# Kernel tuning notes

Measured on AMD Instinct MI355X. Metric: run time of the kernel, lower is better.

## Reference

```python
import jax, jax.numpy as jnp
import numpy as np

N_NODES = 100000


def gcn_conv(x, W, b, src, dst, num_nodes):
    # GCNConv with self-loops and symmetric normalization (PyG defaults).
    h = x @ W  # [N, F_out]
    ones = jnp.ones(src.shape[0], dtype=x.dtype)
    deg = jax.ops.segment_sum(ones, dst, num_segments=num_nodes) + 1.0  # +1 self-loop
    dinv = jax.lax.rsqrt(deg)  # deg^{-1/2}
    norm = dinv[src] * dinv[dst]  # [E]
    msg = h[src] * norm[:, None]  # gather + scale, [E, F_out]
    agg = jax.ops.segment_sum(msg, dst, num_segments=num_nodes)
    agg = agg + h * (dinv * dinv)[:, None]  # self-loop term: dinv[i]*dinv[i]
    return agg + b


def setup_inputs() -> dict:
    key = jax.random.key(0)
    k = jax.random.split(key, 6)
    in_c, hid_c, out_c = 64, 64, 32
    E = 1600000
    x = jax.random.normal(k[0], (N_NODES, in_c), dtype=jnp.float32)
    edge_index = jax.random.randint(k[1], (2, E), 0, N_NODES, dtype=jnp.int32)
    W1 = jax.random.normal(k[2], (in_c, hid_c), dtype=jnp.float32) / np.sqrt(in_c)
    b1 = jnp.zeros((hid_c,), dtype=jnp.float32)
    W2 = jax.random.normal(k[3], (hid_c, out_c), dtype=jnp.float32) / np.sqrt(hid_c)
    b2 = jnp.zeros((out_c,), dtype=jnp.float32)
    return {"x": x, "edge_index": edge_index, "W1": W1, "b1": b1, "W2": W2, "b2": b2}


def reference(x, edge_index, W1, b1, W2, b2):
    src, dst = edge_index[0], edge_index[1]
    h = jax.nn.relu(gcn_conv(x, W1, b1, src, dst, N_NODES))
    # dropout is identity in inference mode
    h = gcn_conv(h, W2, b2, src, dst, N_NODES)
    return jax.nn.log_softmax(h, axis=1)
```

## Files before the change

### kernel.cpp

```cpp
#include <hip/hip_runtime.h>
#include <hip/hip_bf16.h>


constexpr int SCAN_CHUNK = 1024;

__device__ __forceinline__ unsigned short f2bf(float f) {
    unsigned u = __float_as_uint(f);
    return (unsigned short)((u + 0x7FFF + ((u >> 16) & 1)) >> 16);
}
__device__ __forceinline__ float bf2f(unsigned short b) {
    return __uint_as_float((unsigned)b << 16);
}

__global__ __launch_bounds__(256) void k_zero(int* __restrict__ p, int n) {
    int i = blockIdx.x * 256 + threadIdx.x;
    if (i < n) p[i] = 0;
}

__global__ __launch_bounds__(256) void k_hist_rank(const int* __restrict__ dst,
                                                   int* __restrict__ cnt,
                                                   int* __restrict__ rank, int E) {
    int e = blockIdx.x * 256 + threadIdx.x;
    if (e < E) rank[e] = atomicAdd(&cnt[dst[e]], 1);
}

__global__ __launch_bounds__(256) void k_scan1(const int* __restrict__ cnt,
                                               int* __restrict__ bsum, int N) {
    __shared__ int sm[256];
    const int t = threadIdx.x;
    const long base = (long)blockIdx.x * SCAN_CHUNK + t * 4;
    int s = 0;
    #pragma unroll
    for (int k = 0; k < 4; ++k) { long i = base + k; if (i < N) s += cnt[i]; }
    sm[t] = s; __syncthreads();
    for (int off = 128; off > 0; off >>= 1) {
        if (t < off) sm[t] += sm[t + off];
        __syncthreads();
    }
    if (t == 0) bsum[blockIdx.x] = sm[0];
}

__global__ __launch_bounds__(256) void k_scan2(const int* __restrict__ bsum,
                                               int* __restrict__ bofs, int nb) {
    __shared__ int sm[256];
    const int t = threadIdx.x;
    const int v = (t < nb) ? bsum[t] : 0;
    sm[t] = v; __syncthreads();
    for (int off = 1; off < 256; off <<= 1) {
        int u = (t >= off) ? sm[t - off] : 0;
        __syncthreads();
        sm[t] += u;
        __syncthreads();
    }
    if (t < nb) bofs[t] = sm[t] - v;
}

__global__ __launch_bounds__(256) void k_scan3(const int* __restrict__ cnt,
                                               const int* __restrict__ bofs,
                                               int* __restrict__ offs,
                                               float* __restrict__ dinv, int N) {
    __shared__ int sm[256];
    const int t = threadIdx.x;
    const long base = (long)blockIdx.x * SCAN_CHUNK + t * 4;
    int c[4]; int s = 0;
    #pragma unroll
    for (int k = 0; k < 4; ++k) { long i = base + k; c[k] = (i < N) ? cnt[i] : 0; s += c[k]; }
    sm[t] = s; __syncthreads();
    for (int off = 1; off < 256; off <<= 1) {
        int u = (t >= off) ? sm[t - off] : 0;
        __syncthreads();
        sm[t] += u;
        __syncthreads();
    }
    int run = bofs[blockIdx.x] + (sm[t] - s);
    #pragma unroll
    for (int k = 0; k < 4; ++k) {
        long i = base + k;
        if (i < N) {
            offs[i] = run;
            dinv[i] = rsqrtf((float)c[k] + 1.0f);
            run += c[k];
        }
    }
}

__global__ __launch_bounds__(256) void k_fill(const int* __restrict__ src,
                                              const int* __restrict__ dst,
                                              const int* __restrict__ rank,
                                              const int* __restrict__ offs,
                                              int* __restrict__ slots, int E) {
    int e = blockIdx.x * 256 + threadIdx.x;
    if (e >= E) return;
    const int pos = offs[dst[e]] + rank[e];
    __builtin_nontemporal_store(src[e], &slots[pos]);
}

template<int IN_C, int OUT_C, bool TRANS_IN>
__global__ __launch_bounds__(256) void k_mm(const float* __restrict__ A,
                                            const float* __restrict__ W,
                                            const float* __restrict__ bin,
                                            unsigned short* __restrict__ out,
                                            int n_rows) {
    constexpr int C4   = OUT_C / 4;
    constexpr int ROWS = 256 / C4;
    __shared__ float Ws[IN_C][OUT_C];
    __shared__ float xs[ROWS][IN_C + 1];
    __shared__ float bs[IN_C];

    const int tid = threadIdx.x;
    for (int i = tid; i < IN_C * OUT_C; i += 256)
        Ws[i / OUT_C][i % OUT_C] = W[i];
    if (tid < IN_C) bs[tid] = TRANS_IN ? bin[tid] : 0.0f;

    const int c4 = (tid % C4) * 4;
    const int rl = tid / C4;
    const int tiles = (n_rows + ROWS - 1) / ROWS;

    for (int t = blockIdx.x; t < tiles; t += gridDim.x) {
        const int r0 = t * ROWS;
        __syncthreads();
        for (int i = tid; i < ROWS * IN_C; i += 256) {
            int r = i / IN_C, k = i % IN_C;
            float v = 0.0f;
            if (r0 + r < n_rows) {
                v = A[(long)(r0 + r) * IN_C + k];
                if (TRANS_IN) v = fmaxf(v + bs[k], 0.0f);
            }
            xs[r][k] = v;
        }
        __syncthreads();

        float4 acc = {0.f, 0.f, 0.f, 0.f};
        #pragma unroll
        for (int k = 0; k < IN_C; ++k) {
            const float a = xs[rl][k];
            const float4 w4 = *reinterpret_cast<const float4*>(&Ws[k][c4]);
            acc.x += a * w4.x; acc.y += a * w4.y;
            acc.z += a * w4.z; acc.w += a * w4.w;
        }
        const int row = r0 + rl;
        if (row < n_rows) {
            ushort4 o;
            o.x = f2bf(acc.x); o.y = f2bf(acc.y);
            o.z = f2bf(acc.z); o.w = f2bf(acc.w);
            *reinterpret_cast<ushort4*>(&out[(long)row * OUT_C + c4]) = o;
        }
    }
}

__global__ __launch_bounds__(256) void k_agg64(const int* __restrict__ offs,
                                               const int* __restrict__ cnt,
                                               const int* __restrict__ slots,
                                               const float* __restrict__ dinv,
                                               const unsigned short* __restrict__ h,
                                               float* __restrict__ agg, int N) {
    const int wid  = threadIdx.x >> 6;
    const int lane = threadIdx.x & 63;
    const int grp  = lane >> 4;
    const int c4   = (lane & 15) * 4;
    const int node = blockIdx.x * 4 + wid;
    if (node >= N) return;
    const int beg = offs[node], deg = cnt[node];
    const float dd = dinv[node];
    float4 acc = {0.f, 0.f, 0.f, 0.f};
    for (int j0 = 0; j0 < deg; j0 += 64) {
        const int m = min(64, deg - j0);
        int sv = 0; float dv = 0.f;
        if (lane < m) { sv = slots[beg + j0 + lane]; dv = dinv[sv]; }
        #pragma unroll 4
        for (int jj = 0; jj < m; jj += 4) {
            const int idx = jj + grp;
            const int   s = __shfl(sv, idx);
            const float w = __shfl(dv, idx) * dd;
            if (idx < m) {
                const ushort4 hv = *reinterpret_cast<const ushort4*>(&h[(long)s * 64 + c4]);
                acc.x += w * bf2f(hv.x); acc.y += w * bf2f(hv.y);
                acc.z += w * bf2f(hv.z); acc.w += w * bf2f(hv.w);
            }
        }
    }
    #pragma unroll
    for (int off = 16; off <= 32; off <<= 1) {
        acc.x += __shfl_xor(acc.x, off); acc.y += __shfl_xor(acc.y, off);
        acc.z += __shfl_xor(acc.z, off); acc.w += __shfl_xor(acc.w, off);
    }
    if (lane < 16) {
        const ushort4 hv = *reinterpret_cast<const ushort4*>(&h[(long)node * 64 + c4]);
        const float w = dd * dd;
        acc.x += w * bf2f(hv.x); acc.y += w * bf2f(hv.y);
        acc.z += w * bf2f(hv.z); acc.w += w * bf2f(hv.w);
        *reinterpret_cast<float4*>(&agg[(long)node * 64 + c4]) = acc;
    }
}

__global__ __launch_bounds__(256) void k_agg32_lsm(const int* __restrict__ offs,
                                                   const int* __restrict__ cnt,
                                                   const int* __restrict__ slots,
                                                   const float* __restrict__ dinv,
                                                   const unsigned short* __restrict__ h,
                                                   const float* __restrict__ b2,
                                                   float* __restrict__ out, int N) {
    const int wid  = threadIdx.x >> 6;
    const int lane = threadIdx.x & 63;
    const int grp  = lane >> 3;
    const int c4   = (lane & 7) * 4;
    const int node = blockIdx.x * 4 + wid;
    if (node >= N) return;
    const int beg = offs[node], deg = cnt[node];
    const float dd = dinv[node];
    float4 acc = {0.f, 0.f, 0.f, 0.f};
    for (int j0 = 0; j0 < deg; j0 += 64) {
        const int m = min(64, deg - j0);
        int sv = 0; float dv = 0.f;
        if (lane < m) { sv = slots[beg + j0 + lane]; dv = dinv[sv]; }
        #pragma unroll 2
        for (int jj = 0; jj < m; jj += 8) {
            const int idx = jj + grp;
            const int   s = __shfl(sv, idx);
            const float w = __shfl(dv, idx) * dd;
            if (idx < m) {
                const ushort4 hv = *reinterpret_cast<const ushort4*>(&h[(long)s * 32 + c4]);
                acc.x += w * bf2f(hv.x); acc.y += w * bf2f(hv.y);
                acc.z += w * bf2f(hv.z); acc.w += w * bf2f(hv.w);
            }
        }
    }
    #pragma unroll
    for (int off = 8; off <= 32; off <<= 1) {
        acc.x += __shfl_xor(acc.x, off); acc.y += __shfl_xor(acc.y, off);
        acc.z += __shfl_xor(acc.z, off); acc.w += __shfl_xor(acc.w, off);
    }
    const ushort4 hv = *reinterpret_cast<const ushort4*>(&h[(long)node * 32 + c4]);
    const float4 bv = *reinterpret_cast<const float4*>(&b2[c4]);
    const float w = dd * dd;
    float4 v;
    v.x = acc.x + w * bf2f(hv.x) + bv.x; v.y = acc.y + w * bf2f(hv.y) + bv.y;
    v.z = acc.z + w * bf2f(hv.z) + bv.z; v.w = acc.w + w * bf2f(hv.w) + bv.w;
    float mx = fmaxf(fmaxf(v.x, v.y), fmaxf(v.z, v.w));
    #pragma unroll
    for (int off = 1; off < 8; off <<= 1) mx = fmaxf(mx, __shfl_xor(mx, off));
    float4 ev;
    ev.x = __expf(v.x - mx); ev.y = __expf(v.y - mx);
    ev.z = __expf(v.z - mx); ev.w = __expf(v.w - mx);
    float ss = ev.x + ev.y + ev.z + ev.w;
    #pragma unroll
    for (int off = 1; off < 8; off <<= 1) ss += __shfl_xor(ss, off);
    const float lg = mx + __logf(ss);
    if (lane < 8) {
        float4 o;
        o.x = v.x - lg; o.y = v.y - lg; o.z = v.z - lg; o.w = v.w - lg;
        *reinterpret_cast<float4*>(&out[(long)node * 32 + c4]) = o;
    }
}

extern "C" void kernel_launch(void* const* d_in, const int* in_sizes, int n_in,
                              void* d_out, int out_size, void* d_ws, size_t ws_size,
                              hipStream_t stream) {
    const float* x  = (const float*)d_in[0];
    const int*   ei = (const int*)  d_in[1];
    const float* W1 = (const float*)d_in[2];
    const float* b1 = (const float*)d_in[3];
    const float* W2 = (const float*)d_in[4];
    const float* b2 = (const float*)d_in[5];
    float* out = (float*)d_out;

    const int N = in_sizes[0] / 64;
    const int E = in_sizes[1] / 2;
    const int* src = ei;
    const int* dst = ei + E;

    auto align = [](long v) { return (v + 63) & ~63L; };
    char* wsb = (char*)d_ws;
    long o = 0;
    int*   cnt    = (int*)(wsb + o * 4); o = align(o + N);
    int*   offs   = (int*)(wsb + o * 4); o = align(o + N);
    int*   bsum   = (int*)(wsb + o * 4); o = align(o + 256);
    int*   bofs   = (int*)(wsb + o * 4); o = align(o + 256);
    float* dinv   = (float*)(wsb + o * 4); o = align(o + N);
    int*   slots  = (int*)(wsb + o * 4); o = align(o + E);
    unsigned short* h1 = (unsigned short*)(wsb + o * 4); o = align(o + (long)N * 32);
    float* agg1   = (float*)(wsb + o * 4); o = align(o + (long)N * 64);
    unsigned short* h2 = h1;
    int*   rank   = (int*)h1;

    const int B = 256;
    auto cdiv = [](long a, long b) { return (int)((a + b - 1) / b); };
    const int nb = cdiv(N, SCAN_CHUNK);

    k_zero     <<<cdiv(N, B), B, 0, stream>>>(cnt, N);
    k_hist_rank<<<cdiv(E, B), B, 0, stream>>>(dst, cnt, rank, E);
    k_scan1    <<<nb, B, 0, stream>>>(cnt, bsum, N);
    k_scan2    <<<1,  B, 0, stream>>>(bsum, bofs, nb);
    k_scan3    <<<nb, B, 0, stream>>>(cnt, bofs, offs, dinv, N);
    k_fill     <<<cdiv(E, B), B, 0, stream>>>(src, dst, rank, offs, slots, E);

    k_mm<64, 64, false><<<2048, B, 0, stream>>>(x, W1, b1, h1, N);
    k_agg64<<<cdiv(N, 4), B, 0, stream>>>(offs, cnt, slots, dinv, h1, agg1, N);

    k_mm<64, 32, true><<<2048, B, 0, stream>>>(agg1, W2, b1, h2, N);
    k_agg32_lsm<<<cdiv(N, 4), B, 0, stream>>>(offs, cnt, slots, dinv, h2, b2, out, N);
}
```

Measured before the change: 353.8 us.

## Privatize degree histogram into eight copies to reduce atomic contention

The degree histogram is split into eight per-block-group copies, so each edge's atomicAdd targets one of eight counters chosen by block index. The scan kernels sum the copies and write a per-copy offset table, and the fill kernel uses that offset plus the rank to place each source. The aim is to spread contended atomics across more addresses. In exchange the zeroing, scan and offset traffic grows eightfold over N, and each edge in the fill stage does a scattered lookup into an array eight times larger.

```diff
diff --git a/kernel.cpp b/kernel.cpp
--- a/kernel.cpp
+++ b/kernel.cpp
@@ -3,6 +3,7 @@
 
 
 constexpr int SCAN_CHUNK = 1024;
+constexpr int NCPY = 8;
 
 __device__ __forceinline__ unsigned short f2bf(float f) {
     unsigned u = __float_as_uint(f);
@@ -12,26 +13,34 @@
     return __uint_as_float((unsigned)b << 16);
 }
 
-__global__ __launch_bounds__(256) void k_zero(int* __restrict__ p, int n) {
-    int i = blockIdx.x * 256 + threadIdx.x;
+__global__ __launch_bounds__(256) void k_zero(int* __restrict__ p, long n) {
+    long i = (long)blockIdx.x * 256 + threadIdx.x;
     if (i < n) p[i] = 0;
 }
 
-__global__ __launch_bounds__(256) void k_hist_rank(const int* __restrict__ dst,
-                                                   int* __restrict__ cnt,
-                                                   int* __restrict__ rank, int E) {
+__global__ __launch_bounds__(256) void k_hist_rank8(const int* __restrict__ dst,
+                                                    int* __restrict__ cnt8,
+                                                    int* __restrict__ rank,
+                                                    int N, int E) {
     int e = blockIdx.x * 256 + threadIdx.x;
-    if (e < E) rank[e] = atomicAdd(&cnt[dst[e]], 1);
-}
-
-__global__ __launch_bounds__(256) void k_scan1(const int* __restrict__ cnt,
+    if (e >= E) return;
+    const int c = blockIdx.x & (NCPY - 1);
+    rank[e] = atomicAdd(&cnt8[(long)c * N + dst[e]], 1);
+}
+
+__global__ __launch_bounds__(256) void k_scan1(const int* __restrict__ cnt8,
                                                int* __restrict__ bsum, int N) {
     __shared__ int sm[256];
     const int t = threadIdx.x;
     const long base = (long)blockIdx.x * SCAN_CHUNK + t * 4;
     int s = 0;
     #pragma unroll
-    for (int k = 0; k < 4; ++k) { long i = base + k; if (i < N) s += cnt[i]; }
+    for (int k = 0; k < 4; ++k) {
+        long i = base + k;
+        if (i < N)
+            #pragma unroll
+            for (int c = 0; c < NCPY; ++c) s += cnt8[(long)c * N + i];
+    }
     sm[t] = s; __syncthreads();
     for (int off = 128; off > 0; off >>= 1) {
         if (t < off) sm[t] += sm[t + off];
@@ -55,16 +64,26 @@
     if (t < nb) bofs[t] = sm[t] - v;
 }
 
-__global__ __launch_bounds__(256) void k_scan3(const int* __restrict__ cnt,
+__global__ __launch_bounds__(256) void k_scan3(const int* __restrict__ cnt8,
                                                const int* __restrict__ bofs,
                                                int* __restrict__ offs,
+                                               int* __restrict__ deg,
+                                               int* __restrict__ copyoff,
                                                float* __restrict__ dinv, int N) {
     __shared__ int sm[256];
     const int t = threadIdx.x;
     const long base = (long)blockIdx.x * SCAN_CHUNK + t * 4;
-    int c[4]; int s = 0;
-    #pragma unroll
-    for (int k = 0; k < 4; ++k) { long i = base + k; c[k] = (i < N) ? cnt[i] : 0; s += c[k]; }
+    int c8[4][NCPY]; int tot[4]; int s = 0;
+    #pragma unroll
+    for (int k = 0; k < 4; ++k) {
+        long i = base + k; tot[k] = 0;
+        #pragma unroll
+        for (int c = 0; c < NCPY; ++c) {
+            c8[k][c] = (i < N) ? cnt8[(long)c * N + i] : 0;
+            tot[k] += c8[k][c];
+        }
+        s += tot[k];
+    }
     sm[t] = s; __syncthreads();
     for (int off = 1; off < 256; off <<= 1) {
         int u = (t >= off) ? sm[t - off] : 0;
@@ -78,20 +97,26 @@
         long i = base + k;
         if (i < N) {
             offs[i] = run;
-            dinv[i] = rsqrtf((float)c[k] + 1.0f);
-            run += c[k];
-        }
-    }
-}
-
-__global__ __launch_bounds__(256) void k_fill(const int* __restrict__ src,
-                                              const int* __restrict__ dst,
-                                              const int* __restrict__ rank,
-                                              const int* __restrict__ offs,
-                                              int* __restrict__ slots, int E) {
+            deg[i]  = tot[k];
+            dinv[i] = rsqrtf((float)tot[k] + 1.0f);
+            int a = run;
+            #pragma unroll
+            for (int c = 0; c < NCPY; ++c) { copyoff[(long)c * N + i] = a; a += c8[k][c]; }
+            run += tot[k];
+        }
+    }
+}
+
+__global__ __launch_bounds__(256) void k_fill8(const int* __restrict__ src,
+                                               const int* __restrict__ dst,
+                                               const int* __restrict__ rank,
+                                               const int* __restrict__ copyoff,
+                                               int* __restrict__ slots,
+                                               int N, int E) {
     int e = blockIdx.x * 256 + threadIdx.x;
     if (e >= E) return;
-    const int pos = offs[dst[e]] + rank[e];
+    const int c = blockIdx.x & (NCPY - 1);
+    const int pos = copyoff[(long)c * N + dst[e]] + rank[e];
     __builtin_nontemporal_store(src[e], &slots[pos]);
 }
 
@@ -149,7 +174,7 @@
 }
 
 __global__ __launch_bounds__(256) void k_agg64(const int* __restrict__ offs,
-                                               const int* __restrict__ cnt,
+                                               const int* __restrict__ deg,
                                                const int* __restrict__ slots,
                                                const float* __restrict__ dinv,
                                                const unsigned short* __restrict__ h,
@@ -160,11 +185,11 @@
     const int c4   = (lane & 15) * 4;
     const int node = blockIdx.x * 4 + wid;
     if (node >= N) return;
-    const int beg = offs[node], deg = cnt[node];
+    const int beg = offs[node], dg = deg[node];
     const float dd = dinv[node];
     float4 acc = {0.f, 0.f, 0.f, 0.f};
-    for (int j0 = 0; j0 < deg; j0 += 64) {
-        const int m = min(64, deg - j0);
+    for (int j0 = 0; j0 < dg; j0 += 64) {
+        const int m = min(64, dg - j0);
         int sv = 0; float dv = 0.f;
         if (lane < m) { sv = slots[beg + j0 + lane]; dv = dinv[sv]; }
         #pragma unroll 4
@@ -194,7 +219,7 @@
 }
 
 __global__ __launch_bounds__(256) void k_agg32_lsm(const int* __restrict__ offs,
-                                                   const int* __restrict__ cnt,
+                                                   const int* __restrict__ deg,
                                                    const int* __restrict__ slots,
                                                    const float* __restrict__ dinv,
                                                    const unsigned short* __restrict__ h,
@@ -206,11 +231,11 @@
     const int c4   = (lane & 7) * 4;
     const int node = blockIdx.x * 4 + wid;
     if (node >= N) return;
-    const int beg = offs[node], deg = cnt[node];
+    const int beg = offs[node], dg = deg[node];
     const float dd = dinv[node];
     float4 acc = {0.f, 0.f, 0.f, 0.f};
-    for (int j0 = 0; j0 < deg; j0 += 64) {
-        const int m = min(64, deg - j0);
+    for (int j0 = 0; j0 < dg; j0 += 64) {
+        const int m = min(64, dg - j0);
         int sv = 0; float dv = 0.f;
         if (lane < m) { sv = slots[beg + j0 + lane]; dv = dinv[sv]; }
         #pragma unroll 2
@@ -272,31 +297,33 @@
     auto align = [](long v) { return (v + 63) & ~63L; };
     char* wsb = (char*)d_ws;
     long o = 0;
-    int*   cnt    = (int*)(wsb + o * 4); o = align(o + N);
-    int*   offs   = (int*)(wsb + o * 4); o = align(o + N);
-    int*   bsum   = (int*)(wsb + o * 4); o = align(o + 256);
-    int*   bofs   = (int*)(wsb + o * 4); o = align(o + 256);
-    float* dinv   = (float*)(wsb + o * 4); o = align(o + N);
-    int*   slots  = (int*)(wsb + o * 4); o = align(o + E);
+    int*   cnt8    = (int*)(wsb + o * 4); o = align(o + (long)NCPY * N);
+    int*   copyoff = (int*)(wsb + o * 4); o = align(o + (long)NCPY * N);
+    int*   offs    = (int*)(wsb + o * 4); o = align(o + N);
+    int*   deg     = (int*)(wsb + o * 4); o = align(o + N);
+    int*   bsum    = (int*)(wsb + o * 4); o = align(o + 256);
+    int*   bofs    = (int*)(wsb + o * 4); o = align(o + 256);
+    float* dinv    = (float*)(wsb + o * 4); o = align(o + N);
+    int*   slots   = (int*)(wsb + o * 4); o = align(o + E);
     unsigned short* h1 = (unsigned short*)(wsb + o * 4); o = align(o + (long)N * 32);
-    float* agg1   = (float*)(wsb + o * 4); o = align(o + (long)N * 64);
+    float* agg1    = (float*)(wsb + o * 4); o = align(o + (long)N * 64);
     unsigned short* h2 = h1;
-    int*   rank   = (int*)h1;
+    int*   rank    = (int*)h1;
 
     const int B = 256;
     auto cdiv = [](long a, long b) { return (int)((a + b - 1) / b); };
     const int nb = cdiv(N, SCAN_CHUNK);
 
-    k_zero     <<<cdiv(N, B), B, 0, stream>>>(cnt, N);
-    k_hist_rank<<<cdiv(E, B), B, 0, stream>>>(dst, cnt, rank, E);
-    k_scan1    <<<nb, B, 0, stream>>>(cnt, bsum, N);
-    k_scan2    <<<1,  B, 0, stream>>>(bsum, bofs, nb);
-    k_scan3    <<<nb, B, 0, stream>>>(cnt, bofs, offs, dinv, N);
-    k_fill     <<<cdiv(E, B), B, 0, stream>>>(src, dst, rank, offs, slots, E);
+    k_zero      <<<cdiv((long)NCPY * N, B), B, 0, stream>>>(cnt8, (long)NCPY * N);
+    k_hist_rank8<<<cdiv(E, B), B, 0, stream>>>(dst, cnt8, rank, N, E);
+    k_scan1     <<<nb, B, 0, stream>>>(cnt8, bsum, N);
+    k_scan2     <<<1,  B, 0, stream>>>(bsum, bofs, nb);
+    k_scan3     <<<nb, B, 0, stream>>>(cnt8, bofs, offs, deg, copyoff, dinv, N);
+    k_fill8     <<<cdiv(E, B), B, 0, stream>>>(src, dst, rank, copyoff, slots, N, E);
 
     k_mm<64, 64, false><<<2048, B, 0, stream>>>(x, W1, b1, h1, N);
-    k_agg64<<<cdiv(N, 4), B, 0, stream>>>(offs, cnt, slots, dinv, h1, agg1, N);
+    k_agg64<<<cdiv(N, 4), B, 0, stream>>>(offs, deg, slots, dinv, h1, agg1, N);
 
     k_mm<64, 32, true><<<2048, B, 0, stream>>>(agg1, W2, b1, h2, N);
-    k_agg32_lsm<<<cdiv(N, 4), B, 0, stream>>>(offs, cnt, slots, dinv, h2, b2, out, N);
-}
+    k_agg32_lsm<<<cdiv(N, 4), B, 0, stream>>>(offs, deg, slots, dinv, h2, b2, out, N);
+}
```

After: 357.9 us. Within noise of the previous version (+1.1%).

## Replace global-atomic CSR build with two-level bucketed counting sort

Applied to the files above, without the earlier changes.

Builds the destination-sorted CSR with a two-level radix-style sort instead of global atomics per edge. The first level buckets edges by dst>>6 using shared-memory histograms per edge chunk, a transposed scan and a scatter. The second level sorts each 64-node bucket in shared memory, packing the local node id with the source index. This removes the contended global atomicAdd histogram and the random rank/fill writes, at the cost of more kernels and an extra intermediate edge buffer. The packing assumes source ids fit in 17 bits and the scan assumes at most 256 edge chunks and 2048 buckets.

```diff
diff --git a/kernel.cpp b/kernel.cpp
--- a/kernel.cpp
+++ b/kernel.cpp
@@ -2,7 +2,8 @@
 #include <hip/hip_bf16.h>
 
 
-constexpr int SCAN_CHUNK = 1024;
+constexpr int NBP     = 2048;
+constexpr int CHUNK   = 16384;
 
 __device__ __forceinline__ unsigned short f2bf(float f) {
     unsigned u = __float_as_uint(f);
@@ -12,39 +13,60 @@
     return __uint_as_float((unsigned)b << 16);
 }
 
-__global__ __launch_bounds__(256) void k_zero(int* __restrict__ p, int n) {
-    int i = blockIdx.x * 256 + threadIdx.x;
-    if (i < n) p[i] = 0;
-}
-
-__global__ __launch_bounds__(256) void k_hist_rank(const int* __restrict__ dst,
-                                                   int* __restrict__ cnt,
-                                                   int* __restrict__ rank, int E) {
-    int e = blockIdx.x * 256 + threadIdx.x;
-    if (e < E) rank[e] = atomicAdd(&cnt[dst[e]], 1);
-}
-
-__global__ __launch_bounds__(256) void k_scan1(const int* __restrict__ cnt,
-                                               int* __restrict__ bsum, int N) {
+__global__ __launch_bounds__(256) void k_bhist(const int* __restrict__ dst,
+                                               int* __restrict__ counts, int E) {
+    __shared__ int hist[NBP];
+    const int t = threadIdx.x, blk = blockIdx.x;
+    for (int i = t; i < NBP; i += 256) hist[i] = 0;
+    __syncthreads();
+    const long e0 = (long)blk * CHUNK;
+    for (int i = t; i < CHUNK; i += 256) {
+        long e = e0 + i;
+        if (e < E) atomicAdd(&hist[dst[e] >> 6], 1);
+    }
+    __syncthreads();
+    for (int i = t; i < NBP; i += 256) counts[(long)blk * NBP + i] = hist[i];
+}
+
+__global__ __launch_bounds__(256) void k_btot(const int* __restrict__ counts,
+                                              int* __restrict__ total, int nblk) {
     __shared__ int sm[256];
-    const int t = threadIdx.x;
-    const long base = (long)blockIdx.x * SCAN_CHUNK + t * 4;
+    const int t = threadIdx.x, b = blockIdx.x;
     int s = 0;
-    #pragma unroll
-    for (int k = 0; k < 4; ++k) { long i = base + k; if (i < N) s += cnt[i]; }
+    for (int r = t; r < nblk; r += 256) s += counts[(long)r * NBP + b];
     sm[t] = s; __syncthreads();
     for (int off = 128; off > 0; off >>= 1) {
         if (t < off) sm[t] += sm[t + off];
         __syncthreads();
     }
-    if (t == 0) bsum[blockIdx.x] = sm[0];
-}
-
-__global__ __launch_bounds__(256) void k_scan2(const int* __restrict__ bsum,
-                                               int* __restrict__ bofs, int nb) {
+    if (t == 0) total[b] = sm[0];
+}
+
+__global__ __launch_bounds__(256) void k_bscan(const int* __restrict__ total,
+                                               int* __restrict__ bbase) {
     __shared__ int sm[256];
     const int t = threadIdx.x;
-    const int v = (t < nb) ? bsum[t] : 0;
+    int v[NBP / 256]; int s = 0;
+    #pragma unroll
+    for (int k = 0; k < NBP / 256; ++k) { v[k] = total[t * (NBP / 256) + k]; s += v[k]; }
+    sm[t] = s; __syncthreads();
+    for (int off = 1; off < 256; off <<= 1) {
+        int u = (t >= off) ? sm[t - off] : 0;
+        __syncthreads();
+        sm[t] += u;
+        __syncthreads();
+    }
+    int run = sm[t] - s;
+    #pragma unroll
+    for (int k = 0; k < NBP / 256; ++k) { bbase[t * (NBP / 256) + k] = run; run += v[k]; }
+}
+
+__global__ __launch_bounds__(256) void k_bbase(const int* __restrict__ counts,
+                                               const int* __restrict__ bbase,
+                                               int* __restrict__ baseT, int nblk) {
+    __shared__ int sm[256];
+    const int t = threadIdx.x, b = blockIdx.x;
+    const int v = (t < nblk) ? counts[(long)t * NBP + b] : 0;
     sm[t] = v; __syncthreads();
     for (int off = 1; off < 256; off <<= 1) {
         int u = (t >= off) ? sm[t - off] : 0;
@@ -52,47 +74,64 @@
         sm[t] += u;
         __syncthreads();
     }
-    if (t < nb) bofs[t] = sm[t] - v;
-}
-
-__global__ __launch_bounds__(256) void k_scan3(const int* __restrict__ cnt,
-                                               const int* __restrict__ bofs,
-                                               int* __restrict__ offs,
-                                               float* __restrict__ dinv, int N) {
-    __shared__ int sm[256];
+    if (t < nblk) baseT[(long)b * nblk + t] = bbase[b] + sm[t] - v;
+}
+
+__global__ __launch_bounds__(256) void k_bscatter(const int* __restrict__ src,
+                                                  const int* __restrict__ dst,
+                                                  const int* __restrict__ baseT,
+                                                  int* __restrict__ ebuf,
+                                                  int E, int nblk) {
+    __shared__ int cur[NBP];
+    const int t = threadIdx.x, blk = blockIdx.x;
+    for (int i = t; i < NBP; i += 256) cur[i] = baseT[(long)i * nblk + blk];
+    __syncthreads();
+    const long e0 = (long)blk * CHUNK;
+    for (int i = t; i < CHUNK; i += 256) {
+        long e = e0 + i;
+        if (e < E) {
+            const int d = dst[e];
+            const int pos = atomicAdd(&cur[d >> 6], 1);
+            ebuf[pos] = ((d & 63) << 17) | src[e];
+        }
+    }
+}
+
+__global__ __launch_bounds__(256) void k_bcsr(const int* __restrict__ ebuf,
+                                              const int* __restrict__ total,
+                                              const int* __restrict__ bbase,
+                                              int* __restrict__ slots,
+                                              int* __restrict__ offs,
+                                              int* __restrict__ deg,
+                                              float* __restrict__ dinv, int N) {
+    const int b = blockIdx.x;
+    const int node0 = b << 6;
+    if (node0 >= N) return;
     const int t = threadIdx.x;
-    const long base = (long)blockIdx.x * SCAN_CHUNK + t * 4;
-    int c[4]; int s = 0;
-    #pragma unroll
-    for (int k = 0; k < 4; ++k) { long i = base + k; c[k] = (i < N) ? cnt[i] : 0; s += c[k]; }
-    sm[t] = s; __syncthreads();
-    for (int off = 1; off < 256; off <<= 1) {
-        int u = (t >= off) ? sm[t - off] : 0;
-        __syncthreads();
-        sm[t] += u;
-        __syncthreads();
-    }
-    int run = bofs[blockIdx.x] + (sm[t] - s);
-    #pragma unroll
-    for (int k = 0; k < 4; ++k) {
-        long i = base + k;
-        if (i < N) {
-            offs[i] = run;
-            dinv[i] = rsqrtf((float)c[k] + 1.0f);
-            run += c[k];
-        }
-    }
-}
-
-__global__ __launch_bounds__(256) void k_fill(const int* __restrict__ src,
-                                              const int* __restrict__ dst,
-                                              const int* __restrict__ rank,
-                                              const int* __restrict__ offs,
-                                              int* __restrict__ slots, int E) {
-    int e = blockIdx.x * 256 + threadIdx.x;
-    if (e >= E) return;
-    const int pos = offs[dst[e]] + rank[e];
-    __builtin_nontemporal_store(src[e], &slots[pos]);
+    __shared__ int cnt[64], loff[64], cur[64];
+    const int nE = total[b], base = bbase[b];
+    if (t < 64) cnt[t] = 0;
+    __syncthreads();
+    for (int i = t; i < nE; i += 256) atomicAdd(&cnt[ebuf[base + i] >> 17], 1);
+    __syncthreads();
+    if (t == 0) {
+        int r = 0;
+        for (int n = 0; n < 64; ++n) { loff[n] = r; cur[n] = r; r += cnt[n]; }
+    }
+    __syncthreads();
+    for (int i = t; i < nE; i += 256) {
+        const int p = ebuf[base + i];
+        const int pos = atomicAdd(&cur[p >> 17], 1);
+        slots[base + pos] = p & 0x1FFFF;
+    }
+    if (t < 64) {
+        const int node = node0 + t;
+        if (node < N) {
+            offs[node] = base + loff[t];
+            deg[node]  = cnt[t];
+            dinv[node] = rsqrtf((float)cnt[t] + 1.0f);
+        }
+    }
 }
 
 template<int IN_C, int OUT_C, bool TRANS_IN>
@@ -149,7 +188,7 @@
 }
 
 __global__ __launch_bounds__(256) void k_agg64(const int* __restrict__ offs,
-                                               const int* __restrict__ cnt,
+                                               const int* __restrict__ deg,
                                                const int* __restrict__ slots,
                                                const float* __restrict__ dinv,
                                                const unsigned short* __restrict__ h,
@@ -160,11 +199,11 @@
     const int c4   = (lane & 15) * 4;
     const int node = blockIdx.x * 4 + wid;
     if (node >= N) return;
-    const int beg = offs[node], deg = cnt[node];
+    const int beg = offs[node], dg = deg[node];
     const float dd = dinv[node];
     float4 acc = {0.f, 0.f, 0.f, 0.f};
-    for (int j0 = 0; j0 < deg; j0 += 64) {
-        const int m = min(64, deg - j0);
+    for (int j0 = 0; j0 < dg; j0 += 64) {
+        const int m = min(64, dg - j0);
         int sv = 0; float dv = 0.f;
         if (lane < m) { sv = slots[beg + j0 + lane]; dv = dinv[sv]; }
         #pragma unroll 4
@@ -194,7 +233,7 @@
 }
 
 __global__ __launch_bounds__(256) void k_agg32_lsm(const int* __restrict__ offs,
-                                                   const int* __restrict__ cnt,
+                                                   const int* __restrict__ deg,
                                                    const int* __restrict__ slots,
                                                    const float* __restrict__ dinv,
                                                    const unsigned short* __restrict__ h,
@@ -206,11 +245,11 @@
     const int c4   = (lane & 7) * 4;
     const int node = blockIdx.x * 4 + wid;
     if (node >= N) return;
-    const int beg = offs[node], deg = cnt[node];
+    const int beg = offs[node], dg = deg[node];
     const float dd = dinv[node];
     float4 acc = {0.f, 0.f, 0.f, 0.f};
-    for (int j0 = 0; j0 < deg; j0 += 64) {
-        const int m = min(64, deg - j0);
+    for (int j0 = 0; j0 < dg; j0 += 64) {
+        const int m = min(64, dg - j0);
         int sv = 0; float dv = 0.f;
         if (lane < m) { sv = slots[beg + j0 + lane]; dv = dinv[sv]; }
         #pragma unroll 2
@@ -269,34 +308,37 @@
     const int* src = ei;
     const int* dst = ei + E;
 
+    auto cdiv = [](long a, long b) { return (int)((a + b - 1) / b); };
+    const int nblk = cdiv(E, CHUNK);
+
     auto align = [](long v) { return (v + 63) & ~63L; };
     char* wsb = (char*)d_ws;
     long o = 0;
-    int*   cnt    = (int*)(wsb + o * 4); o = align(o + N);
+    int*   counts = (int*)(wsb + o * 4); o = align(o + (long)nblk * NBP);
+    int*   total  = (int*)(wsb + o * 4); o = align(o + NBP);
+    int*   bbase  = (int*)(wsb + o * 4); o = align(o + NBP);
+    int*   baseT  = (int*)(wsb + o * 4); o = align(o + (long)NBP * nblk);
+    int*   ebuf   = (int*)(wsb + o * 4); o = align(o + E);
+    int*   slots  = (int*)(wsb + o * 4); o = align(o + E);
     int*   offs   = (int*)(wsb + o * 4); o = align(o + N);
-    int*   bsum   = (int*)(wsb + o * 4); o = align(o + 256);
-    int*   bofs   = (int*)(wsb + o * 4); o = align(o + 256);
+    int*   deg    = (int*)(wsb + o * 4); o = align(o + N);
     float* dinv   = (float*)(wsb + o * 4); o = align(o + N);
-    int*   slots  = (int*)(wsb + o * 4); o = align(o + E);
     unsigned short* h1 = (unsigned short*)(wsb + o * 4); o = align(o + (long)N * 32);
     float* agg1   = (float*)(wsb + o * 4); o = align(o + (long)N * 64);
     unsigned short* h2 = h1;
-    int*   rank   = (int*)h1;
 
     const int B = 256;
-    auto cdiv = [](long a, long b) { return (int)((a + b - 1) / b); };
-    const int nb = cdiv(N, SCAN_CHUNK);
-
-    k_zero     <<<cdiv(N, B), B, 0, stream>>>(cnt, N);
-    k_hist_rank<<<cdiv(E, B), B, 0, stream>>>(dst, cnt, rank, E);
-    k_scan1    <<<nb, B, 0, stream>>>(cnt, bsum, N);
-    k_scan2    <<<1,  B, 0, stream>>>(bsum, bofs, nb);
-    k_scan3    <<<nb, B, 0, stream>>>(cnt, bofs, offs, dinv, N);
-    k_fill     <<<cdiv(E, B), B, 0, stream>>>(src, dst, rank, offs, slots, E);
+
+    k_bhist   <<<nblk, B, 0, stream>>>(dst, counts, E);
+    k_btot    <<<NBP,  B, 0, stream>>>(counts, total, nblk);
+    k_bscan   <<<1,    B, 0, stream>>>(total, bbase);
+    k_bbase   <<<NBP,  B, 0, stream>>>(counts, bbase, baseT, nblk);
+    k_bscatter<<<nblk, B, 0, stream>>>(src, dst, baseT, ebuf, E, nblk);
+    k_bcsr    <<<NBP,  B, 0, stream>>>(ebuf, total, bbase, slots, offs, deg, dinv, N);
 
     k_mm<64, 64, false><<<2048, B, 0, stream>>>(x, W1, b1, h1, N);
-    k_agg64<<<cdiv(N, 4), B, 0, stream>>>(offs, cnt, slots, dinv, h1, agg1, N);
+    k_agg64<<<cdiv(N, 4), B, 0, stream>>>(offs, deg, slots, dinv, h1, agg1, N);
 
     k_mm<64, 32, true><<<2048, B, 0, stream>>>(agg1, W2, b1, h2, N);
-    k_agg32_lsm<<<cdiv(N, 4), B, 0, stream>>>(offs, cnt, slots, dinv, h2, b2, out, N);
-}
+    k_agg32_lsm<<<cdiv(N, 4), B, 0, stream>>>(offs, deg, slots, dinv, h2, b2, out, N);
+}
```

Result: faster. 312.1 us (-11.8%).
